# Kernel optimization log

Measured on AMD Instinct MI355X. Metric: run time of the kernel, lower is better.

The kernel has to match this reference:

```python
import jax, jax.numpy as jnp
import numpy as np

BN_EPS = 1e-5
DIST_EPS = 1e-8


def setup_inputs() -> dict:
    key = jax.random.key(0)
    ks = jax.random.split(key, 10)
    B, Ni, Mi = 4, 16384, 4096
    C1, C2 = 64, 64
    Cin = C1 + C2  # 128, mlp=[128,128,128]
    inp = {
        "unknown": jax.random.normal(ks[0], (B * Ni, 3), dtype=jnp.float32),
        "unknown_batch_cnt": np.full(B, Ni, dtype=np.int64),
        "known": jax.random.normal(ks[1], (B * Mi, 3), dtype=jnp.float32),
        "known_batch_cnt": np.full(B, Mi, dtype=np.int64),
        "unknown_feats": jax.random.normal(ks[2], (B * Ni, C1), dtype=jnp.float32),
        "known_feats": jax.random.normal(ks[3], (B * Mi, C2), dtype=jnp.float32),
        "W1": jax.random.normal(ks[4], (128, Cin), dtype=jnp.float32) * 0.05,
        "g1": jnp.ones((128,), dtype=jnp.float32),
        "b1": jnp.zeros((128,), dtype=jnp.float32),
        "W2": jax.random.normal(ks[5], (128, 128), dtype=jnp.float32) * 0.05,
        "g2": jnp.ones((128,), dtype=jnp.float32),
        "b2": jnp.zeros((128,), dtype=jnp.float32),
    }
    return inp


def _three_nn(u, k):
    # u: (B,Ni,3), k: (B,Mi,3) -> dist (B,Ni,3), idx (B,Ni,3) within each batch
    d2 = (jnp.sum(u * u, -1)[:, :, None] + jnp.sum(k * k, -1)[:, None, :]
          - 2.0 * jnp.einsum("bnd,bmd->bnm", u, k))  # (B,Ni,Mi)
    neg_d2, idx = jax.lax.top_k(-d2, 3)
    dist = jnp.sqrt(jnp.maximum(-neg_d2, 0.0))
    return dist, idx


def _bn_relu(y, g, b):
    # BatchNorm2d over the point dim (training-mode batch stats), then ReLU
    mu = jnp.mean(y, axis=0)
    var = jnp.mean((y - mu) ** 2, axis=0)
    return jax.nn.relu((y - mu) * jax.lax.rsqrt(var + BN_EPS) * g + b)


def reference(unknown, unknown_batch_cnt, known, known_batch_cnt,
              unknown_feats, known_feats, W1, g1, b1, W2, g2, b2):
    ucnt = np.asarray(unknown_batch_cnt)
    kcnt = np.asarray(known_batch_cnt)
    B = ucnt.shape[0]
    Ni, Mi = int(ucnt[0]), int(kcnt[0])  # equal-count ragged batches
    C2 = known_feats.shape[1]

    u = unknown.reshape(B, Ni, 3)
    k = known.reshape(B, Mi, 3)
    dist, idx = _three_nn(u, k)

    dist_recip = 1.0 / (dist + DIST_EPS)
    weight = dist_recip / jnp.sum(dist_recip, axis=-1, keepdims=True)  # (B,Ni,3)

    kf = known_feats.reshape(B, Mi, C2)
    gathered = kf[jnp.arange(B)[:, None, None], idx]  # (B,Ni,3,C2)
    interp = jnp.sum(weight[..., None] * gathered, axis=2).reshape(B * Ni, C2)

    x = jnp.concatenate([interp, unknown_feats], axis=1)  # (N, C2+C1)
    x = _bn_relu(x @ W1.T, g1, b1)
    x = _bn_relu(x @ W2.T, g2, b2)
    return x
```

## Files before the change

kernel.cpp:

```cpp
#include <hip/hip_runtime.h>
#include <hip/hip_bf16.h>

#define GRID  32
#define NCELL (GRID * GRID * GRID)
#define H     0.3125f
#define INVH  3.2f
#define OFF   5.0f
#define SUBW  8
#define XPAD  136
#define NREP  16

using f32x4  = __attribute__((ext_vector_type(4))) float;
using bf16x8 = __attribute__((ext_vector_type(8))) short;

static __device__ inline short f2bs(float f) {
  __hip_bfloat16 h = __float2bfloat16(f);
  return __builtin_bit_cast(short, h);
}
static __device__ inline float bs2f(short s) {
  return __bfloat162float(__builtin_bit_cast(__hip_bfloat16, s));
}
static __device__ inline int cellco(float x) {
  int c = (int)((x + OFF) * INVH);
  return min(GRID - 1, max(0, c));
}

#define INS3(B0, B1, B2, J0, J1, J2, dv, mv)           \
  {                                                    \
    bool q0 = dv < B0, q1 = dv < B1, q2 = dv < B2;     \
    float P0 = B0, P1 = B1; int Q0 = J0, Q1 = J1;      \
    B2 = q1 ? P1 : (q2 ? dv : B2);                     \
    J2 = q1 ? Q1 : (q2 ? mv : J2);                     \
    B1 = q0 ? P0 : (q1 ? dv : P1);                     \
    J1 = q0 ? Q0 : (q1 ? mv : Q1);                     \
    B0 = q0 ? dv : P0;                                 \
    J0 = q0 ? mv : Q0;                                 \
  }
#define INSF(dv, mv) INS3(b0, b1, b2, j0, j1, j2, dv, mv)

#define MERGE3(lo_mk, hi_mk)                                                        \
  for (int mk = lo_mk; mk <= hi_mk; mk <<= 1) {                                     \
    float ob0 = __shfl_xor(b0, mk), ob1 = __shfl_xor(b1, mk), ob2 = __shfl_xor(b2, mk); \
    int   oj0 = __shfl_xor(j0, mk), oj1 = __shfl_xor(j1, mk), oj2 = __shfl_xor(j2, mk); \
    INSF(ob0, oj0); INSF(ob1, oj1); INSF(ob2, oj2);                                 \
  }

__global__ __launch_bounds__(256) void zero_k(int4* __restrict__ dst, int n4) {
  int i = blockIdx.x * 256 + threadIdx.x;
  if (i < n4) dst[i] = int4{0, 0, 0, 0};
}

__global__ __launch_bounds__(256) void hist_k(
    const float* __restrict__ known, int Mtot, int Mi,
    const float* __restrict__ unknown, int Ntot,
    int* __restrict__ khist, int* __restrict__ qhist,
    int* __restrict__ kcell, int* __restrict__ qcell,
    const float* __restrict__ W1, const float* __restrict__ W2,
    __hip_bfloat16* __restrict__ Wb1, __hip_bfloat16* __restrict__ Wb2) {
  int i = blockIdx.x * 256 + threadIdx.x;
  if (i < 128 * 128) {
    Wb1[i] = __float2bfloat16(W1[i]);
    Wb2[i] = __float2bfloat16(W2[i]);
  }
  if (i < Mtot) {
    int b = i / Mi;
    float x = known[(size_t)i * 3], y = known[(size_t)i * 3 + 1], z = known[(size_t)i * 3 + 2];
    int c = b * NCELL + (cellco(z) * GRID + cellco(y)) * GRID + cellco(x);
    kcell[i] = c;
    atomicAdd(&khist[c], 1);
  }
  if (i < Ntot) {
    int Ni = Ntot / (Mtot / Mi);
    int b = i / Ni;
    float x = unknown[(size_t)i * 3], y = unknown[(size_t)i * 3 + 1], z = unknown[(size_t)i * 3 + 2];
    int c = b * NCELL + (cellco(z) * GRID + cellco(y)) * GRID + cellco(x);
    qcell[i] = c;
    atomicAdd(&qhist[c], 1);
  }
}

__global__ __launch_bounds__(256) void scan1_k(
    const int4* __restrict__ Hc4, int* __restrict__ bsum) {
  __shared__ int sh[256];
  int t = threadIdx.x;
  int4 h = Hc4[blockIdx.x * 256 + t];
  int s = h.x + h.y + h.z + h.w;
  sh[t] = s;
  __syncthreads();
  for (int d = 128; d > 0; d >>= 1) {
    if (t < d) sh[t] += sh[t + d];
    __syncthreads();
  }
  if (t == 0) bsum[blockIdx.x] = sh[0];
}

__global__ __launch_bounds__(256) void scan3_k(
    const int4* __restrict__ Hc4, const int* __restrict__ bsum, int nbk,
    int* __restrict__ kstart, int* __restrict__ kfill,
    int* __restrict__ qstart, int* __restrict__ qfill,
    int nc, int Mtot, int Ntot) {
  __shared__ int sh[256];
  __shared__ int sv[256], sc[256];
  int t = threadIdx.x;
  int v = (t < nbk) ? bsum[t] : 0;
  sv[t] = v; sc[t] = v;
  int g4 = blockIdx.x * 256 + t;
  int4 h = Hc4[g4];
  int s = h.x + h.y + h.z + h.w;
  sh[t] = s;
  __syncthreads();
  for (int d = 1; d < 256; d <<= 1) {
    int u1 = (t >= d) ? sc[t - d] : 0;
    int u2 = (t >= d) ? sh[t - d] : 0;
    __syncthreads();
    sc[t] += u1;
    sh[t] += u2;
    __syncthreads();
  }
  int blockbase = sc[blockIdx.x] - sv[blockIdx.x];
  int run = blockbase + sh[t] - s;
  int hv[4] = {h.x, h.y, h.z, h.w};
#pragma unroll
  for (int j = 0; j < 4; ++j) {
    int g = g4 * 4 + j;
    if (g < nc) { kstart[g] = run; kfill[g] = run; }
    else        { int q = g - nc; qstart[q] = run - Mtot; qfill[q] = run - Mtot; }
    run += hv[j];
  }
  if (blockIdx.x == 0 && t == 0) { kstart[nc] = Mtot; qstart[nc] = Ntot; }
}

__global__ __launch_bounds__(256) void scatter_k(
    const float* __restrict__ known, int Mtot, int Mi,
    const float* __restrict__ unknown, int Ntot,
    const int* __restrict__ kcell, const int* __restrict__ qcell,
    int* __restrict__ kfill, int* __restrict__ qfill,
    f32x4* __restrict__ k4s, int* __restrict__ korder,
    f32x4* __restrict__ u4s, int* __restrict__ qorder) {
  int i = blockIdx.x * 256 + threadIdx.x;
  if (i < Mtot) {
    int slot = atomicAdd(&kfill[kcell[i]], 1);
    float x = known[(size_t)i * 3], y = known[(size_t)i * 3 + 1], z = known[(size_t)i * 3 + 2];
    f32x4 v;
    v[0] = -2.f * x; v[1] = -2.f * y; v[2] = -2.f * z;
    v[3] = x * x + y * y + z * z;
    k4s[slot] = v;
    korder[slot] = i - (i / Mi) * Mi;
  }
  if (i < Ntot) {
    int slot = atomicAdd(&qfill[qcell[i]], 1);
    float x = unknown[(size_t)i * 3], y = unknown[(size_t)i * 3 + 1], z = unknown[(size_t)i * 3 + 2];
    f32x4 v;
    v[0] = x; v[1] = y; v[2] = z;
    v[3] = __fmaf_rn(x, x, __fmaf_rn(y, y, z * z));
    u4s[slot] = v;
    qorder[slot] = i;
  }
}

static __device__ __forceinline__ void scan_box_strided(
    int R, int sub, int stride, int cx, int cy, int cz, int cellbase,
    const int* __restrict__ cstart, const f32x4* __restrict__ k4s,
    const int* __restrict__ korder,
    float ux, float uy, float uz,
    float& b0, float& b1, float& b2, int& j0, int& j1, int& j2) {
  int zlo = max(cz - R, 0), zhi = min(cz + R, GRID - 1);
  int ylo = max(cy - R, 0), yhi = min(cy + R, GRID - 1);
  int xlo = max(cx - R, 0), xhi = min(cx + R, GRID - 1);
  int ny = yhi - ylo + 1;
  int nrows = (zhi - zlo + 1) * ny;
  for (int rid = sub; rid < nrows; rid += stride) {
    int zz = rid / ny;
    int y  = ylo + (rid - zz * ny);
    int row = cellbase + ((zlo + zz) * GRID + y) * GRID;
    int s = cstart[row + xlo];
    int e = cstart[row + xhi + 1];
    for (int i = s; i < e; ++i) {
      f32x4 k = k4s[i];
      float d = __fmaf_rn(ux, k[0], __fmaf_rn(uy, k[1], __fmaf_rn(uz, k[2], k[3])));
      int m = korder[i];
      INSF(d, m);
    }
  }
}

__global__ __launch_bounds__(256) void knn_grid_k(
    const f32x4* __restrict__ u4s, const int* __restrict__ qorder,
    const int* __restrict__ cstart, const f32x4* __restrict__ k4s,
    const int* __restrict__ korder, int Ni,
    float* __restrict__ w, int* __restrict__ idx,
    int* __restrict__ rcnt, int* __restrict__ rlist, float* __restrict__ rd3) {
  int nwc = gridDim.x * 4;
  int gw  = blockIdx.x * 4 + (threadIdx.x >> 6);
  int wchunk = (gw * 997) & (nwc - 1);
  int s   = wchunk * 8 + ((threadIdx.x & 63) / SUBW);
  int sub = threadIdx.x & (SUBW - 1);
  f32x4 u4 = u4s[s];
  int p = qorder[s];
  int b = p / Ni;
  float ux = u4[0], uy = u4[1], uz = u4[2], uu = u4[3];
  int cx = cellco(ux), cy = cellco(uy), cz = cellco(uz);
  int cellbase = b * NCELL;
  int xlo = max(cx - 1, 0), xhi = min(cx + 1, GRID - 1);

  float fx = (ux + OFF) * INVH - cx;
  float fy = (uy + OFF) * INVH - cy;
  float fz = (uz + OFF) * INVH - cz;
  float mf = fminf(fminf(fminf(fx, 1.f - fx), fminf(fy, 1.f - fy)),
                   fminf(fz, 1.f - fz));
  float cov = H * (1.f + fmaxf(mf, 0.f));
  float covsq = cov * cov;

  int cs[9], ce[9];
#pragma unroll
  for (int q = 0; q < 9; ++q) {
    int z = cz + (q / 3) - 1;
    int y = cy + (q % 3) - 1;
    bool valid = ((unsigned)z < GRID) && ((unsigned)y < GRID);
    int row = cellbase + (z * GRID + y) * GRID;
    int a0 = valid ? row + xlo : cellbase;
    int a1 = valid ? row + xhi + 1 : cellbase;
    cs[q] = cstart[a0];
    ce[q] = cstart[a1];
  }

  float b0 = 3e38f, b1 = 3e38f, b2 = 3e38f;
  int   j0 = 0,     j1 = 0,     j2 = 0;
  float e0 = 3e38f, e1 = 3e38f, e2 = 3e38f;
  int   f0 = 0,     f1 = 0,     f2 = 0;
#pragma unroll
  for (int q = 0; q < 9; ++q) {
    int i = cs[q] + sub;
    int e = ce[q];
    for (; i + SUBW < e; i += 2 * SUBW) {
      f32x4 kA = k4s[i];
      f32x4 kB = k4s[i + SUBW];
      int mA = korder[i];
      int mB = korder[i + SUBW];
      float dA = __fmaf_rn(ux, kA[0], __fmaf_rn(uy, kA[1], __fmaf_rn(uz, kA[2], kA[3])));
      float dB = __fmaf_rn(ux, kB[0], __fmaf_rn(uy, kB[1], __fmaf_rn(uz, kB[2], kB[3])));
      INS3(b0, b1, b2, j0, j1, j2, dA, mA);
      INS3(e0, e1, e2, f0, f1, f2, dB, mB);
    }
    if (i < e) {
      f32x4 kA = k4s[i];
      int mA = korder[i];
      float dA = __fmaf_rn(ux, kA[0], __fmaf_rn(uy, kA[1], __fmaf_rn(uz, kA[2], kA[3])));
      INS3(b0, b1, b2, j0, j1, j2, dA, mA);
    }
  }
  INSF(e0, f0); INSF(e1, f1); INSF(e2, f2);
  MERGE3(1, SUBW / 2);

  float d3sq = b2 + uu;
  bool ok = d3sq <= covsq;

  if (sub == 0) {
    if (ok) {
      float d0 = sqrtf(fmaxf(b0 + uu, 0.f));
      float d1 = sqrtf(fmaxf(b1 + uu, 0.f));
      float d2 = sqrtf(fmaxf(b2 + uu, 0.f));
      float r0 = 1.f / (d0 + 1e-8f);
      float r1 = 1.f / (d1 + 1e-8f);
      float r2 = 1.f / (d2 + 1e-8f);
      float rs = 1.f / (r0 + r1 + r2);
      size_t o = (size_t)p * 3;
      w[o] = r0 * rs; w[o + 1] = r1 * rs; w[o + 2] = r2 * rs;
      idx[o] = j0; idx[o + 1] = j1; idx[o + 2] = j2;
    } else {
      int t = atomicAdd(rcnt, 1);
      rlist[t] = s;
      rd3[t] = d3sq;
    }
  }
}

__global__ __launch_bounds__(256) void knn_retry_k(
    const f32x4* __restrict__ u4s, const int* __restrict__ qorder,
    const int* __restrict__ rlist, const float* __restrict__ rd3,
    const int* __restrict__ rcnt,
    const int* __restrict__ cstart, const f32x4* __restrict__ k4s,
    const int* __restrict__ korder, int Ni,
    float* __restrict__ w, int* __restrict__ idx) {
  int lane = threadIdx.x & 63;
  int wv   = blockIdx.x * 4 + (threadIdx.x >> 6);
  int nw   = gridDim.x * 4;
  int cnt  = rcnt[0];
  for (int q = wv; q < cnt; q += nw) {
    int sq = rlist[q];
    f32x4 u4 = u4s[sq];
    int p = qorder[sq];
    int b = p / Ni;
    float ux = u4[0], uy = u4[1], uz = u4[2], uu = u4[3];
    int cx = cellco(ux), cy = cellco(uy), cz = cellco(uz);
    int cellbase = b * NCELL;

    float d3sq = rd3[q];
    int Rc = 1;
    float b0, b1, b2; int j0, j1, j2;
    bool ok = false;
    while (!ok) {
      if (d3sq < 1e30f) {
        Rc = max((int)ceilf(sqrtf(fmaxf(d3sq, 0.f)) * INVH), Rc + 1);
      } else {
        Rc = Rc * 2;
      }
      Rc = min(Rc, GRID);
      b0 = b1 = b2 = 3e38f; j0 = j1 = j2 = 0;
      scan_box_strided(Rc, lane, 64, cx, cy, cz, cellbase, cstart, k4s, korder,
                       ux, uy, uz, b0, b1, b2, j0, j1, j2);
      MERGE3(1, 32);
      d3sq = b2 + uu;
      float cov = (float)Rc * H;
      ok = (d3sq <= cov * cov) || (Rc >= GRID);
    }
    if (lane == 0) {
      float d0 = sqrtf(fmaxf(b0 + uu, 0.f));
      float d1 = sqrtf(fmaxf(b1 + uu, 0.f));
      float d2 = sqrtf(fmaxf(b2 + uu, 0.f));
      float r0 = 1.f / (d0 + 1e-8f);
      float r1 = 1.f / (d1 + 1e-8f);
      float r2 = 1.f / (d2 + 1e-8f);
      float rs = 1.f / (r0 + r1 + r2);
      size_t o = (size_t)p * 3;
      w[o] = r0 * rs; w[o + 1] = r1 * rs; w[o + 2] = r2 * rs;
      idx[o] = j0; idx[o + 1] = j1; idx[o + 2] = j2;
    }
  }
}

template <bool F32OUT>
static __device__ __forceinline__ void gemm_half(
    const short* xs, const short* Ws, int row0,
    float* yf, __hip_bfloat16* yb, float* ls, float* lq) {
  int t = threadIdx.x;
  int lane = t & 63;
  int wv = t >> 6;
  int r = lane & 15, g = lane >> 4;
  int tile = wv >> 1, half = wv & 1;
  int trow = tile * 16;

  bf16x8 a[4];
#pragma unroll
  for (int q = 0; q < 4; ++q)
    a[q] = *reinterpret_cast<const bf16x8*>(&xs[(trow + r) * XPAD + g * 8 + q * 32]);

  int orow = row0 + trow + g * 4;
#pragma unroll
  for (int ct = 0; ct < 4; ++ct) {
    int ocol = half * 64 + ct * 16 + r;
    f32x4 acc = {0.f, 0.f, 0.f, 0.f};
    size_t bbase = (size_t)ocol * 128 + g * 8;
#pragma unroll
    for (int q = 0; q < 4; ++q) {
      bf16x8 bfr = *reinterpret_cast<const bf16x8*>(Ws + bbase + q * 32);
      acc = __builtin_amdgcn_mfma_f32_16x16x32_bf16(a[q], bfr, acc, 0, 0, 0);
    }
    if (F32OUT) {
#pragma unroll
      for (int i = 0; i < 4; ++i)
        yf[(size_t)(orow + i) * 128 + ocol] = acc[i];
    } else {
#pragma unroll
      for (int i = 0; i < 4; ++i)
        yb[(size_t)(orow + i) * 128 + ocol] = __float2bfloat16(acc[i]);
    }
    float s  = acc[0] + acc[1] + acc[2] + acc[3];
    float q2 = acc[0] * acc[0] + acc[1] * acc[1] + acc[2] * acc[2] + acc[3] * acc[3];
    s  += __shfl_xor(s, 16);  s  += __shfl_xor(s, 32);
    q2 += __shfl_xor(q2, 16); q2 += __shfl_xor(q2, 32);
    if (g == 0) {
      atomicAdd(&ls[ocol], s);
      atomicAdd(&lq[ocol], q2);
    }
  }
}

__global__ __launch_bounds__(256) void gemm1_fused_k(
    const float* __restrict__ kf, const float* __restrict__ uf,
    const float* __restrict__ wgt, const int* __restrict__ idx,
    const __hip_bfloat16* __restrict__ Wb, __hip_bfloat16* __restrict__ Yb,
    float* __restrict__ stats, int Ni, int Mi) {
  __shared__ short xs[32 * XPAD];
  __shared__ float ls[128], lq[128];
  int t = threadIdx.x;
  if (t < 128) { ls[t] = 0.f; lq[t] = 0.f; }
  int row0 = blockIdx.x * 32;

  int rr = t >> 3, c0 = (t & 7) * 16;
  int p = row0 + rr;
  short tmp[16];
  if (c0 < 64) {
    size_t o = (size_t)p * 3;
    float w0 = wgt[o], w1 = wgt[o + 1], w2 = wgt[o + 2];
    int i0 = idx[o], i1 = idx[o + 1], i2 = idx[o + 2];
    int b = p / Ni;
    const float* kfb = kf + (size_t)b * Mi * 64 + c0;
    const f32x4* r0p = reinterpret_cast<const f32x4*>(kfb + (size_t)i0 * 64);
    const f32x4* r1p = reinterpret_cast<const f32x4*>(kfb + (size_t)i1 * 64);
    const f32x4* r2p = reinterpret_cast<const f32x4*>(kfb + (size_t)i2 * 64);
#pragma unroll
    for (int j = 0; j < 4; ++j) {
      f32x4 av = r0p[j], bv = r1p[j], cv = r2p[j];
#pragma unroll
      for (int e = 0; e < 4; ++e)
        tmp[j * 4 + e] = f2bs(w0 * av[e] + w1 * bv[e] + w2 * cv[e]);
    }
  } else {
    const f32x4* ufp = reinterpret_cast<const f32x4*>(uf + (size_t)p * 64 + (c0 - 64));
#pragma unroll
    for (int j = 0; j < 4; ++j) {
      f32x4 av = ufp[j];
#pragma unroll
      for (int e = 0; e < 4; ++e)
        tmp[j * 4 + e] = f2bs(av[e]);
    }
  }
  *reinterpret_cast<bf16x8*>(&xs[rr * XPAD + c0])     = *reinterpret_cast<bf16x8*>(&tmp[0]);
  *reinterpret_cast<bf16x8*>(&xs[rr * XPAD + c0 + 8]) = *reinterpret_cast<bf16x8*>(&tmp[8]);
  __syncthreads();

  gemm_half<false>(xs, reinterpret_cast<const short*>(Wb), row0, nullptr, Yb, ls, lq);

  __syncthreads();
  if (t < 128) {
    int rep = blockIdx.x & (NREP - 1);
    atomicAdd(&stats[rep * 256 + t], ls[t]);
    atomicAdd(&stats[rep * 256 + 128 + t], lq[t]);
  }
}

__global__ __launch_bounds__(256) void gemm2_bn_k(
    const __hip_bfloat16* __restrict__ Y1, const float* __restrict__ AB,
    const __hip_bfloat16* __restrict__ Wb, __hip_bfloat16* __restrict__ Yb2,
    float* __restrict__ stats) {
  __shared__ short xs[32 * XPAD];
  __shared__ float ls[128], lq[128];
  int t = threadIdx.x;
  if (t < 128) { ls[t] = 0.f; lq[t] = 0.f; }
  int row0 = blockIdx.x * 32;

  int rr = t >> 3, c0 = (t & 7) * 16;
  int p = row0 + rr;
  const short* Ys = reinterpret_cast<const short*>(Y1);
  bf16x8 v0 = *reinterpret_cast<const bf16x8*>(Ys + (size_t)p * 128 + c0);
  bf16x8 v1 = *reinterpret_cast<const bf16x8*>(Ys + (size_t)p * 128 + c0 + 8);
  short tmp[16];
#pragma unroll
  for (int j = 0; j < 8; ++j)
    tmp[j] = f2bs(fmaxf(bs2f(v0[j]) * AB[c0 + j] + AB[128 + c0 + j], 0.f));
#pragma unroll
  for (int j = 0; j < 8; ++j)
    tmp[8 + j] = f2bs(fmaxf(bs2f(v1[j]) * AB[c0 + 8 + j] + AB[128 + c0 + 8 + j], 0.f));
  *reinterpret_cast<bf16x8*>(&xs[rr * XPAD + c0])     = *reinterpret_cast<bf16x8*>(&tmp[0]);
  *reinterpret_cast<bf16x8*>(&xs[rr * XPAD + c0 + 8]) = *reinterpret_cast<bf16x8*>(&tmp[8]);
  __syncthreads();

  gemm_half<false>(xs, reinterpret_cast<const short*>(Wb), row0, nullptr, Yb2, ls, lq);

  __syncthreads();
  if (t < 128) {
    int rep = blockIdx.x & (NREP - 1);
    atomicAdd(&stats[rep * 256 + t], ls[t]);
    atomicAdd(&stats[rep * 256 + 128 + t], lq[t]);
  }
}

__global__ void finalize_k(const float* __restrict__ stats, const float* __restrict__ g,
                           const float* __restrict__ bb, float invN, float* __restrict__ AB) {
  int c = threadIdx.x;
  float s = 0.f, q = 0.f;
  for (int rpl = 0; rpl < NREP; ++rpl) {
    s += stats[rpl * 256 + c];
    q += stats[rpl * 256 + 128 + c];
  }
  float mu  = s * invN;
  float var = q * invN - mu * mu;
  float A = rsqrtf(var + 1e-5f) * g[c];
  AB[c] = A;
  AB[128 + c] = bb[c] - mu * A;
}

__global__ __launch_bounds__(256) void bnrelu_out_k(
    const __hip_bfloat16* __restrict__ Y, const float* __restrict__ AB,
    float* __restrict__ Out, long n8) {
  long i = (long)blockIdx.x * 256 + threadIdx.x;
  long stride = (long)gridDim.x * 256;
  const bf16x8* Y8 = reinterpret_cast<const bf16x8*>(Y);
  for (; i < n8; i += stride) {
    bf16x8 y = Y8[i];
    int c0 = (int)((i * 8) & 127);
    f32x4 o0, o1;
#pragma unroll
    for (int j = 0; j < 4; ++j)
      o0[j] = fmaxf(bs2f(y[j]) * AB[c0 + j] + AB[128 + c0 + j], 0.f);
#pragma unroll
    for (int j = 0; j < 4; ++j)
      o1[j] = fmaxf(bs2f(y[4 + j]) * AB[c0 + 4 + j] + AB[128 + c0 + 4 + j], 0.f);
    reinterpret_cast<f32x4*>(Out)[i * 2]     = o0;
    reinterpret_cast<f32x4*>(Out)[i * 2 + 1] = o1;
  }
}

extern "C" void kernel_launch(void* const* d_in, const int* in_sizes, int n_in,
                              void* d_out, int out_size, void* d_ws, size_t ws_size,
                              hipStream_t stream) {
  const float* unknown = (const float*)d_in[0];
  const float* known   = (const float*)d_in[2];
  const float* uf      = (const float*)d_in[4];
  const float* kf      = (const float*)d_in[5];
  const float* W1      = (const float*)d_in[6];
  const float* g1      = (const float*)d_in[7];
  const float* b1      = (const float*)d_in[8];
  const float* W2      = (const float*)d_in[9];
  const float* g2      = (const float*)d_in[10];
  const float* b2      = (const float*)d_in[11];

  int B    = in_sizes[1];
  int Ntot = in_sizes[0] / 3;
  int Mtot = in_sizes[2] / 3;
  int Ni = Ntot / B, Mi = Mtot / B;
  int nc = B * NCELL;
  int n2 = 2 * nc;

  char* ws = (char*)d_ws;
  size_t off = 0;
  auto alloc = [&](size_t bytes) {
    void* p = ws + off;
    off += (bytes + 255) & ~(size_t)255;
    return p;
  };
  float* stats  = (float*)alloc(2 * NREP * 256 * 4);
  int*   rcnt   = (int*)alloc(4);
  int*   khist  = (int*)alloc((size_t)n2 * 4);
  int*   qhist  = khist + nc;
  size_t zero_bytes = (size_t)((char*)(khist + n2) - (char*)stats);
  int*   kstart = (int*)alloc((size_t)(nc + 1) * 4);
  int*   qstart = (int*)alloc((size_t)(nc + 1) * 4);
  int*   kfill  = (int*)alloc((size_t)nc * 4);
  int*   qfill  = (int*)alloc((size_t)nc * 4);
  int*   kcell  = (int*)alloc((size_t)Mtot * 4);
  int*   qcell  = (int*)alloc((size_t)Ntot * 4);
  int*   korder = (int*)alloc((size_t)Mtot * 4);
  int*   qorder = (int*)alloc((size_t)Ntot * 4);
  int*   bsum   = (int*)alloc((size_t)(n2 / 1024) * 4);
  int*   rlist  = (int*)alloc((size_t)Ntot * 4);
  float* rd3    = (float*)alloc((size_t)Ntot * 4);
  f32x4* k4s    = (f32x4*)alloc((size_t)Mtot * 16);
  f32x4* u4s    = (f32x4*)alloc((size_t)Ntot * 16);
  float* wgt    = (float*)alloc((size_t)Ntot * 3 * 4);
  int*   idx    = (int*)alloc((size_t)Ntot * 3 * 4);
  __hip_bfloat16* y1b = (__hip_bfloat16*)alloc((size_t)Ntot * 128 * 2);
  __hip_bfloat16* y2b = (__hip_bfloat16*)alloc((size_t)Ntot * 128 * 2);
  __hip_bfloat16* Wb1 = (__hip_bfloat16*)alloc(128 * 128 * 2);
  __hip_bfloat16* Wb2 = (__hip_bfloat16*)alloc(128 * 128 * 2);
  float* AB1 = (float*)alloc(256 * 4);
  float* AB2 = (float*)alloc(256 * 4);

  float* y2 = (float*)d_out;
  long n8 = (long)Ntot * 128 / 8;
  float invN = 1.0f / (float)Ntot;
  int nb = n2 / 1024;
  float* stats2 = stats + NREP * 256;
  int zn4 = (int)(zero_bytes / 16);

  zero_k<<<(zn4 + 255) / 256, 256, 0, stream>>>((int4*)stats, zn4);
  hist_k<<<(Ntot + 255) / 256, 256, 0, stream>>>(known, Mtot, Mi, unknown, Ntot,
                                                 khist, qhist, kcell, qcell, W1, W2, Wb1, Wb2);
  scan1_k<<<nb, 256, 0, stream>>>((const int4*)khist, bsum);
  scan3_k<<<nb, 256, 0, stream>>>((const int4*)khist, bsum, nb, kstart, kfill,
                                  qstart, qfill, nc, Mtot, Ntot);
  scatter_k<<<(Ntot + 255) / 256, 256, 0, stream>>>(known, Mtot, Mi, unknown, Ntot,
                                                    kcell, qcell, kfill, qfill, k4s, korder, u4s, qorder);
  knn_grid_k<<<Ntot / 32, 256, 0, stream>>>(u4s, qorder, kstart, k4s, korder, Ni,
                                            wgt, idx, rcnt, rlist, rd3);
  knn_retry_k<<<1024, 256, 0, stream>>>(u4s, qorder, rlist, rd3, rcnt,
                                        kstart, k4s, korder, Ni, wgt, idx);
  gemm1_fused_k<<<Ntot / 32, 256, 0, stream>>>(kf, uf, wgt, idx, Wb1, y1b, stats, Ni, Mi);
  finalize_k<<<1, 128, 0, stream>>>(stats, g1, b1, invN, AB1);
  gemm2_bn_k<<<Ntot / 32, 256, 0, stream>>>(y1b, AB1, Wb2, y2b, stats2);
  finalize_k<<<1, 128, 0, stream>>>(stats2, g2, b2, invN, AB2);
  bnrelu_out_k<<<2048, 256, 0, stream>>>(y2b, AB2, y2, n8);
}
```

Measured before the change: 149.2 us.

## Inline KNN retry into grid kernel and fold BN finalize into consumers

The separate retry kernel is removed. Queries whose grid search is not yet certain are now handled in the same wave: the whole wave cooperatively rescans a larger box for each failing query, one after another. The two single-block finalize kernels are also removed, and every block of the following kernel recomputes the BN scale and shift from the replicated stats into shared memory. This cuts three kernel launches plus the atomic retry list. In exchange, waves with a failing query stall the other lanes, and the stats reduction is repeated in each block.

New measurement: 168.0 us. 1.13x slower.

```diff
diff --git a/kernel.cpp b/kernel.cpp
--- a/kernel.cpp
+++ b/kernel.cpp
@@ -184,16 +184,31 @@
   }
 }
 
+static __device__ __forceinline__ void write_result(
+    float* __restrict__ w, int* __restrict__ idx, int p, float uu,
+    float b0, float b1, float b2, int j0, int j1, int j2) {
+  float d0 = sqrtf(fmaxf(b0 + uu, 0.f));
+  float d1 = sqrtf(fmaxf(b1 + uu, 0.f));
+  float d2 = sqrtf(fmaxf(b2 + uu, 0.f));
+  float r0 = 1.f / (d0 + 1e-8f);
+  float r1 = 1.f / (d1 + 1e-8f);
+  float r2 = 1.f / (d2 + 1e-8f);
+  float rs = 1.f / (r0 + r1 + r2);
+  size_t o = (size_t)p * 3;
+  w[o] = r0 * rs; w[o + 1] = r1 * rs; w[o + 2] = r2 * rs;
+  idx[o] = j0; idx[o + 1] = j1; idx[o + 2] = j2;
+}
+
 __global__ __launch_bounds__(256) void knn_grid_k(
     const f32x4* __restrict__ u4s, const int* __restrict__ qorder,
     const int* __restrict__ cstart, const f32x4* __restrict__ k4s,
     const int* __restrict__ korder, int Ni,
-    float* __restrict__ w, int* __restrict__ idx,
-    int* __restrict__ rcnt, int* __restrict__ rlist, float* __restrict__ rd3) {
+    float* __restrict__ w, int* __restrict__ idx) {
   int nwc = gridDim.x * 4;
   int gw  = blockIdx.x * 4 + (threadIdx.x >> 6);
   int wchunk = (gw * 997) & (nwc - 1);
-  int s   = wchunk * 8 + ((threadIdx.x & 63) / SUBW);
+  int lane = threadIdx.x & 63;
+  int s   = wchunk * 8 + (lane / SUBW);
   int sub = threadIdx.x & (SUBW - 1);
   f32x4 u4 = u4s[s];
   int p = qorder[s];
@@ -255,77 +270,46 @@
   float d3sq = b2 + uu;
   bool ok = d3sq <= covsq;
 
-  if (sub == 0) {
-    if (ok) {
-      float d0 = sqrtf(fmaxf(b0 + uu, 0.f));
-      float d1 = sqrtf(fmaxf(b1 + uu, 0.f));
-      float d2 = sqrtf(fmaxf(b2 + uu, 0.f));
-      float r0 = 1.f / (d0 + 1e-8f);
-      float r1 = 1.f / (d1 + 1e-8f);
-      float r2 = 1.f / (d2 + 1e-8f);
-      float rs = 1.f / (r0 + r1 + r2);
-      size_t o = (size_t)p * 3;
-      w[o] = r0 * rs; w[o + 1] = r1 * rs; w[o + 2] = r2 * rs;
-      idx[o] = j0; idx[o + 1] = j1; idx[o + 2] = j2;
-    } else {
-      int t = atomicAdd(rcnt, 1);
-      rlist[t] = s;
-      rd3[t] = d3sq;
-    }
-  }
-}
-
-__global__ __launch_bounds__(256) void knn_retry_k(
-    const f32x4* __restrict__ u4s, const int* __restrict__ qorder,
-    const int* __restrict__ rlist, const float* __restrict__ rd3,
-    const int* __restrict__ rcnt,
-    const int* __restrict__ cstart, const f32x4* __restrict__ k4s,
-    const int* __restrict__ korder, int Ni,
-    float* __restrict__ w, int* __restrict__ idx) {
-  int lane = threadIdx.x & 63;
-  int wv   = blockIdx.x * 4 + (threadIdx.x >> 6);
-  int nw   = gridDim.x * 4;
-  int cnt  = rcnt[0];
-  for (int q = wv; q < cnt; q += nw) {
-    int sq = rlist[q];
-    f32x4 u4 = u4s[sq];
-    int p = qorder[sq];
-    int b = p / Ni;
-    float ux = u4[0], uy = u4[1], uz = u4[2], uu = u4[3];
-    int cx = cellco(ux), cy = cellco(uy), cz = cellco(uz);
-    int cellbase = b * NCELL;
-
-    float d3sq = rd3[q];
+  if (ok && sub == 0)
+    write_result(w, idx, p, uu, b0, b1, b2, j0, j1, j2);
+
+  unsigned long long mask = __ballot(!ok && sub == 0);
+  while (mask) {
+    int leader = __ffsll((long long)mask) - 1;
+    mask &= mask - 1;
+    float qux = __shfl(ux, leader);
+    float quy = __shfl(uy, leader);
+    float quz = __shfl(uz, leader);
+    float quu = __shfl(uu, leader);
+    float dd  = __shfl(d3sq, leader);
+    int   qp  = __shfl(p, leader);
+    int qb = qp / Ni;
+    int qcx = cellco(qux), qcy = cellco(quy), qcz = cellco(quz);
+    int qcb = qb * NCELL;
     int Rc = 1;
-    float b0, b1, b2; int j0, j1, j2;
-    bool ok = false;
-    while (!ok) {
-      if (d3sq < 1e30f) {
-        Rc = max((int)ceilf(sqrtf(fmaxf(d3sq, 0.f)) * INVH), Rc + 1);
+    bool done = false;
+    float B0, B1, B2; int J0, J1, J2;
+    while (!done) {
+      if (dd < 1e30f) {
+        Rc = max((int)ceilf(sqrtf(fmaxf(dd, 0.f)) * INVH), Rc + 1);
       } else {
         Rc = Rc * 2;
       }
       Rc = min(Rc, GRID);
-      b0 = b1 = b2 = 3e38f; j0 = j1 = j2 = 0;
-      scan_box_strided(Rc, lane, 64, cx, cy, cz, cellbase, cstart, k4s, korder,
-                       ux, uy, uz, b0, b1, b2, j0, j1, j2);
-      MERGE3(1, 32);
-      d3sq = b2 + uu;
-      float cov = (float)Rc * H;
-      ok = (d3sq <= cov * cov) || (Rc >= GRID);
-    }
-    if (lane == 0) {
-      float d0 = sqrtf(fmaxf(b0 + uu, 0.f));
-      float d1 = sqrtf(fmaxf(b1 + uu, 0.f));
-      float d2 = sqrtf(fmaxf(b2 + uu, 0.f));
-      float r0 = 1.f / (d0 + 1e-8f);
-      float r1 = 1.f / (d1 + 1e-8f);
-      float r2 = 1.f / (d2 + 1e-8f);
-      float rs = 1.f / (r0 + r1 + r2);
-      size_t o = (size_t)p * 3;
-      w[o] = r0 * rs; w[o + 1] = r1 * rs; w[o + 2] = r2 * rs;
-      idx[o] = j0; idx[o + 1] = j1; idx[o + 2] = j2;
-    }
+      {
+        float b0 = 3e38f, b1 = 3e38f, b2 = 3e38f;
+        int   j0 = 0,     j1 = 0,     j2 = 0;
+        scan_box_strided(Rc, lane, 64, qcx, qcy, qcz, qcb, cstart, k4s, korder,
+                         qux, quy, quz, b0, b1, b2, j0, j1, j2);
+        MERGE3(1, 32);
+        B0 = b0; B1 = b1; B2 = b2; J0 = j0; J1 = j1; J2 = j2;
+      }
+      dd = B2 + quu;
+      float cv = (float)Rc * H;
+      done = (dd <= cv * cv) || (Rc >= GRID);
+    }
+    if (lane == 0)
+      write_result(w, idx, qp, quu, B0, B1, B2, J0, J1, J2);
   }
 }
 
@@ -431,13 +415,29 @@
 }
 
 __global__ __launch_bounds__(256) void gemm2_bn_k(
-    const __hip_bfloat16* __restrict__ Y1, const float* __restrict__ AB,
+    const __hip_bfloat16* __restrict__ Y1, const float* __restrict__ stats,
+    const float* __restrict__ g1, const float* __restrict__ b1v, float invN,
     const __hip_bfloat16* __restrict__ Wb, __hip_bfloat16* __restrict__ Yb2,
-    float* __restrict__ stats) {
+    float* __restrict__ stats2) {
   __shared__ short xs[32 * XPAD];
   __shared__ float ls[128], lq[128];
+  __shared__ float ABs[256];
   int t = threadIdx.x;
-  if (t < 128) { ls[t] = 0.f; lq[t] = 0.f; }
+  if (t < 128) {
+    float s = 0.f, q = 0.f;
+#pragma unroll
+    for (int rpl = 0; rpl < NREP; ++rpl) {
+      s += stats[rpl * 256 + t];
+      q += stats[rpl * 256 + 128 + t];
+    }
+    float mu  = s * invN;
+    float var = q * invN - mu * mu;
+    float A = rsqrtf(var + 1e-5f) * g1[t];
+    ABs[t] = A;
+    ABs[128 + t] = b1v[t] - mu * A;
+    ls[t] = 0.f; lq[t] = 0.f;
+  }
+  __syncthreads();
   int row0 = blockIdx.x * 32;
 
   int rr = t >> 3, c0 = (t & 7) * 16;
@@ -448,10 +448,10 @@
   short tmp[16];
 #pragma unroll
   for (int j = 0; j < 8; ++j)
-    tmp[j] = f2bs(fmaxf(bs2f(v0[j]) * AB[c0 + j] + AB[128 + c0 + j], 0.f));
+    tmp[j] = f2bs(fmaxf(bs2f(v0[j]) * ABs[c0 + j] + ABs[128 + c0 + j], 0.f));
 #pragma unroll
   for (int j = 0; j < 8; ++j)
-    tmp[8 + j] = f2bs(fmaxf(bs2f(v1[j]) * AB[c0 + 8 + j] + AB[128 + c0 + 8 + j], 0.f));
+    tmp[8 + j] = f2bs(fmaxf(bs2f(v1[j]) * ABs[c0 + 8 + j] + ABs[128 + c0 + 8 + j], 0.f));
   *reinterpret_cast<bf16x8*>(&xs[rr * XPAD + c0])     = *reinterpret_cast<bf16x8*>(&tmp[0]);
   *reinterpret_cast<bf16x8*>(&xs[rr * XPAD + c0 + 8]) = *reinterpret_cast<bf16x8*>(&tmp[8]);
   __syncthreads();
@@ -461,30 +461,32 @@
   __syncthreads();
   if (t < 128) {
     int rep = blockIdx.x & (NREP - 1);
-    atomicAdd(&stats[rep * 256 + t], ls[t]);
-    atomicAdd(&stats[rep * 256 + 128 + t], lq[t]);
-  }
-}
-
-__global__ void finalize_k(const float* __restrict__ stats, const float* __restrict__ g,
-                           const float* __restrict__ bb, float invN, float* __restrict__ AB) {
-  int c = threadIdx.x;
-  float s = 0.f, q = 0.f;
-  for (int rpl = 0; rpl < NREP; ++rpl) {
-    s += stats[rpl * 256 + c];
-    q += stats[rpl * 256 + 128 + c];
-  }
-  float mu  = s * invN;
-  float var = q * invN - mu * mu;
-  float A = rsqrtf(var + 1e-5f) * g[c];
-  AB[c] = A;
-  AB[128 + c] = bb[c] - mu * A;
+    atomicAdd(&stats2[rep * 256 + t], ls[t]);
+    atomicAdd(&stats2[rep * 256 + 128 + t], lq[t]);
+  }
 }
 
 __global__ __launch_bounds__(256) void bnrelu_out_k(
-    const __hip_bfloat16* __restrict__ Y, const float* __restrict__ AB,
+    const __hip_bfloat16* __restrict__ Y, const float* __restrict__ stats2,
+    const float* __restrict__ g2, const float* __restrict__ b2v, float invN,
     float* __restrict__ Out, long n8) {
-  long i = (long)blockIdx.x * 256 + threadIdx.x;
+  __shared__ float ABs[256];
+  int t = threadIdx.x;
+  if (t < 128) {
+    float s = 0.f, q = 0.f;
+#pragma unroll
+    for (int rpl = 0; rpl < NREP; ++rpl) {
+      s += stats2[rpl * 256 + t];
+      q += stats2[rpl * 256 + 128 + t];
+    }
+    float mu  = s * invN;
+    float var = q * invN - mu * mu;
+    float A = rsqrtf(var + 1e-5f) * g2[t];
+    ABs[t] = A;
+    ABs[128 + t] = b2v[t] - mu * A;
+  }
+  __syncthreads();
+  long i = (long)blockIdx.x * 256 + t;
   long stride = (long)gridDim.x * 256;
   const bf16x8* Y8 = reinterpret_cast<const bf16x8*>(Y);
   for (; i < n8; i += stride) {
@@ -493,10 +495,10 @@
     f32x4 o0, o1;
 #pragma unroll
     for (int j = 0; j < 4; ++j)
-      o0[j] = fmaxf(bs2f(y[j]) * AB[c0 + j] + AB[128 + c0 + j], 0.f);
+      o0[j] = fmaxf(bs2f(y[j]) * ABs[c0 + j] + ABs[128 + c0 + j], 0.f);
 #pragma unroll
     for (int j = 0; j < 4; ++j)
-      o1[j] = fmaxf(bs2f(y[4 + j]) * AB[c0 + 4 + j] + AB[128 + c0 + 4 + j], 0.f);
+      o1[j] = fmaxf(bs2f(y[4 + j]) * ABs[c0 + 4 + j] + ABs[128 + c0 + 4 + j], 0.f);
     reinterpret_cast<f32x4*>(Out)[i * 2]     = o0;
     reinterpret_cast<f32x4*>(Out)[i * 2 + 1] = o1;
   }
@@ -531,7 +533,6 @@
     return p;
   };
   float* stats  = (float*)alloc(2 * NREP * 256 * 4);
-  int*   rcnt   = (int*)alloc(4);
   int*   khist  = (int*)alloc((size_t)n2 * 4);
   int*   qhist  = khist + nc;
   size_t zero_bytes = (size_t)((char*)(khist + n2) - (char*)stats);
@@ -544,8 +545,6 @@
   int*   korder = (int*)alloc((size_t)Mtot * 4);
   int*   qorder = (int*)alloc((size_t)Ntot * 4);
   int*   bsum   = (int*)alloc((size_t)(n2 / 1024) * 4);
-  int*   rlist  = (int*)alloc((size_t)Ntot * 4);
-  float* rd3    = (float*)alloc((size_t)Ntot * 4);
   f32x4* k4s    = (f32x4*)alloc((size_t)Mtot * 16);
   f32x4* u4s    = (f32x4*)alloc((size_t)Ntot * 16);
   float* wgt    = (float*)alloc((size_t)Ntot * 3 * 4);
@@ -554,8 +553,6 @@
   __hip_bfloat16* y2b = (__hip_bfloat16*)alloc((size_t)Ntot * 128 * 2);
   __hip_bfloat16* Wb1 = (__hip_bfloat16*)alloc(128 * 128 * 2);
   __hip_bfloat16* Wb2 = (__hip_bfloat16*)alloc(128 * 128 * 2);
-  float* AB1 = (float*)alloc(256 * 4);
-  float* AB2 = (float*)alloc(256 * 4);
 
   float* y2 = (float*)d_out;
   long n8 = (long)Ntot * 128 / 8;
@@ -572,13 +569,8 @@
                                   qstart, qfill, nc, Mtot, Ntot);
   scatter_k<<<(Ntot + 255) / 256, 256, 0, stream>>>(known, Mtot, Mi, unknown, Ntot,
                                                     kcell, qcell, kfill, qfill, k4s, korder, u4s, qorder);
-  knn_grid_k<<<Ntot / 32, 256, 0, stream>>>(u4s, qorder, kstart, k4s, korder, Ni,
-                                            wgt, idx, rcnt, rlist, rd3);
-  knn_retry_k<<<1024, 256, 0, stream>>>(u4s, qorder, rlist, rd3, rcnt,
-                                        kstart, k4s, korder, Ni, wgt, idx);
+  knn_grid_k<<<Ntot / 32, 256, 0, stream>>>(u4s, qorder, kstart, k4s, korder, Ni, wgt, idx);
   gemm1_fused_k<<<Ntot / 32, 256, 0, stream>>>(kf, uf, wgt, idx, Wb1, y1b, stats, Ni, Mi);
-  finalize_k<<<1, 128, 0, stream>>>(stats, g1, b1, invN, AB1);
-  gemm2_bn_k<<<Ntot / 32, 256, 0, stream>>>(y1b, AB1, Wb2, y2b, stats2);
-  finalize_k<<<1, 128, 0, stream>>>(stats2, g2, b2, invN, AB2);
-  bnrelu_out_k<<<2048, 256, 0, stream>>>(y2b, AB2, y2, n8);
-}
+  gemm2_bn_k<<<Ntot / 32, 256, 0, stream>>>(y1b, stats, g1, b1, invN, Wb2, y2b, stats2);
+  bnrelu_out_k<<<2048, 256, 0, stream>>>(y2b, stats2, g2, b2, invN, y2, n8);
+}
```
